# Optimization experiments

Measured on AMD Instinct MI355X. Metric: run time of the kernel, lower is better.

Reference implementation:

```python
import jax, jax.numpy as jnp
import numpy as np

B, H, S, F_RANK, D_HEAD = 1, 8, 4096, 64, 64
NEG = -1e9


def setup_inputs() -> dict:
    key = jax.random.key(0)
    k1, k2, k3, k4 = jax.random.split(key, 4)
    v = jax.random.normal(k1, (B, H, S, D_HEAD), dtype=jnp.float32)
    A1 = jax.random.normal(k2, (B, H, S, F_RANK), dtype=jnp.float32)
    A2 = jax.random.normal(k3, (B, H, F_RANK, S), dtype=jnp.float32)
    mask = jax.random.randint(k4, (B, 1, S, S), 0, 2, dtype=jnp.int32)
    return {"v": v, "A1": A1, "A2": A2, "mask": mask, "len_q": S}


def reference(v, A1, A2, mask, len_q):
    # Rank-f factorized scores: [B,H,len_q,len_q]
    scores = jnp.einsum('bhsf,bhft->bhst', A1[:, :, :len_q, :], A2[:, :, :, :len_q])
    scores = scores[:mask.shape[0]]
    # masked_fill(mask != 0, -1e9)
    scores = jnp.where(mask[:, :, :len_q, :len_q] != 0, jnp.float32(NEG), scores)
    attn = jax.nn.softmax(scores, axis=-1)  # dropout is identity in eval mode
    output = jnp.einsum('bhst,bhtd->bhsd', attn, v[:, :, :len_q, :])
    return (output, attn)
```

## Files before the change

### kernel.cpp

```cpp
#include <hip/hip_runtime.h>
#include <hip/hip_bf16.h>
#include <stdint.h>

#define S_LEN 4096
#define NHEAD 8
#define NEGV  (-1000000000.0f)
#define L2E   1.44269504088896340736f

typedef __attribute__((ext_vector_type(8))) short bf16x8;
typedef __attribute__((ext_vector_type(4))) float f32x4;
typedef unsigned short u16;
typedef unsigned int   u32;

#define MFMA16(a,b,c) __builtin_amdgcn_mfma_f32_16x16x32_bf16((a),(b),(c),0,0,0)
#define EXP2F(x) __builtin_amdgcn_exp2f((x))

__device__ __forceinline__ void gl_lds16(const void* g, void* l) {
  __builtin_amdgcn_global_load_lds((const __attribute__((address_space(1))) void*)g,
                                   (__attribute__((address_space(3))) void*)l, 16, 0, 0);
}

#define WS_A1HI 0u
#define WS_A1LO (4u<<20)
#define WS_A2HI (8u<<20)
#define WS_A2LO (12u<<20)
#define WS_VHI  (16u<<20)
#define WS_VLO  (20u<<20)
#define WS_BM   (24u<<20)

__global__ void pk_mask(const int* __restrict__ mask, u32* __restrict__ bmT) {
  const int sb = blockIdx.x >> 4;
  const int t  = (blockIdx.x & 15) * 256 + threadIdx.x;
  u32 w = 0;
  #pragma unroll
  for (int j = 0; j < 32; ++j)
    w |= (mask[(size_t)(sb * 32 + j) * S_LEN + t] != 0 ? 1u : 0u) << j;
  bmT[sb * S_LEN + t] = w;
}

__global__ void pk_split(const float* __restrict__ src, u16* __restrict__ hi, u16* __restrict__ lo) {
  const int i = blockIdx.x * 256 + threadIdx.x;
  float4 x = ((const float4*)src)[i];
  ushort4 hv, lv;
  #pragma unroll
  for (int j = 0; j < 4; ++j) {
    float xv = ((const float*)&x)[j];
    __hip_bfloat16 hb = __float2bfloat16(xv);
    float hf = __bfloat162float(hb);
    __hip_bfloat16 lb = __float2bfloat16(xv - hf);
    ((u16*)&hv)[j] = *(u16*)&hb;
    ((u16*)&lv)[j] = *(u16*)&lb;
  }
  ((ushort4*)hi)[i] = hv;
  ((ushort4*)lo)[i] = lv;
}

__global__ void pk_tsplit(const float* __restrict__ src, u16* __restrict__ hi, u16* __restrict__ lo,
                          int chunk_stride, int row_stride) {
  const int h = blockIdx.x >> 6, ci = blockIdx.x & 63;
  const float* base = src + (size_t)h * (S_LEN * 64) + (size_t)ci * chunk_stride;
  __shared__ float tile[64][65];
  const int jr = threadIdx.x & 63, ir = threadIdx.x >> 6;
  #pragma unroll
  for (int p = 0; p < 16; ++p) {
    int i = p * 4 + ir;
    tile[i][jr] = base[(size_t)i * row_stride + jr];
  }
  __syncthreads();
  const size_t ob = (size_t)(h * 64 + ci) * 4096;
  #pragma unroll
  for (int p = 0; p < 16; ++p) {
    int o = p * 256 + threadIdx.x;
    int r = o >> 6;
    int cc = (o & 63) ^ ((r & 7) << 3);
    float xv = tile[cc][r];
    __hip_bfloat16 hb = __float2bfloat16(xv);
    float hf = __bfloat162float(hb);
    __hip_bfloat16 lb = __float2bfloat16(xv - hf);
    hi[ob + o] = *(u16*)&hb;
    lo[ob + o] = *(u16*)&lb;
  }
}

__launch_bounds__(256, 2)
__global__ void fattn_main(const u16* __restrict__ a1hi, const u16* __restrict__ a1lo,
                           const u16* __restrict__ a2hi, const u16* __restrict__ a2lo,
                           const u16* __restrict__ vhi,  const u16* __restrict__ vlo,
                           const u32* __restrict__ bmT,  float* __restrict__ dout) {
  constexpr int TB = 128, NCH = S_LEN / TB;
  const int h   = blockIdx.x & 7;
  const int sb  = blockIdx.x >> 3;
  const int tid = threadIdx.x;
  const int w = tid >> 6, lane = tid & 63;
  const int g = lane >> 4, c = lane & 15;
  const int wsr = w >> 1;
  const int wth = w & 1;
  const int sbase = sb * 64 + wsr * 32;
  const int sb32  = sb * 2 + wsr;

  __shared__ __align__(16) char smem[76800];
  u16* st_a2h = (u16*)smem;
  u16* st_a2l = (u16*)(smem + 16384);
  u16* st_vh  = (u16*)(smem + 32768);
  u16* st_vl  = (u16*)(smem + 49152);
  u16* atb    = (u16*)(smem + 65536);
  float* mlm  = (float*)(smem + 75776);
  float* mll  = (float*)(smem + 75776 + 512);

  bf16x8 a1f[2][2][2];
  #pragma unroll
  for (int mt = 0; mt < 2; ++mt)
    #pragma unroll
    for (int kk = 0; kk < 2; ++kk) {
      size_t base = (size_t)(h * S_LEN + sbase + mt * 16 + c) * 64 + kk * 32 + g * 8;
      a1f[mt][kk][0] = *(const bf16x8*)(a1hi + base);
      a1f[mt][kk][1] = *(const bf16x8*)(a1lo + base);
    }

  float rm[2][4], rl[2][4];
  #pragma unroll
  for (int mt = 0; mt < 2; ++mt)
    #pragma unroll
    for (int r = 0; r < 4; ++r) { rm[mt][r] = -INFINITY; rl[mt][r] = 0.f; }

  const u32* bmrow = bmT + (size_t)sb32 * S_LEN;

  auto stage16 = [&](u16* dst, const u16* srcb) {
    const char* gsb = (const char*)srcb;
    #pragma unroll
    for (int i = 0; i < 4; ++i) {
      int blk = i * 4 + w;
      gl_lds16(gsb + blk * 1024 + lane * 16, (char*)dst + blk * 1024);
    }
  };

  auto compute_scores = [&](f32x4 (&acc)[2][4]) {
    #pragma unroll
    for (int kk = 0; kk < 2; ++kk)
      #pragma unroll
      for (int nt = 0; nt < 4; ++nt) {
        int eb = wth * 4096 + (nt * 16 + c) * 64 + ((kk * 32 + g * 8) ^ ((c & 7) << 3));
        bf16x8 bh = *(const bf16x8*)(st_a2h + eb);
        bf16x8 bl = *(const bf16x8*)(st_a2l + eb);
        #pragma unroll
        for (int mt = 0; mt < 2; ++mt) {
          acc[mt][nt] = MFMA16(a1f[mt][kk][0], bh, acc[mt][nt]);
          acc[mt][nt] = MFMA16(a1f[mt][kk][0], bl, acc[mt][nt]);
          acc[mt][nt] = MFMA16(a1f[mt][kk][1], bh, acc[mt][nt]);
        }
      }
  };

  #pragma unroll 1
  for (int ci = 0; ci < NCH; ++ci) {
    __syncthreads();
    stage16(st_a2h, a2hi + (size_t)(h * 64 + ci * 2) * 4096);
    stage16(st_a2l, a2lo + (size_t)(h * 64 + ci * 2) * 4096);
    __syncthreads();

    f32x4 acc[2][4];
    #pragma unroll
    for (int mt = 0; mt < 2; ++mt)
      #pragma unroll
      for (int nt = 0; nt < 4; ++nt) acc[mt][nt] = (f32x4){0.f, 0.f, 0.f, 0.f};
    compute_scores(acc);

    u32 mw[4];
    #pragma unroll
    for (int nt = 0; nt < 4; ++nt) mw[nt] = bmrow[ci * TB + wth * 64 + nt * 16 + c];

    float x[2][4][4];
    #pragma unroll
    for (int mt = 0; mt < 2; ++mt)
      #pragma unroll
      for (int nt = 0; nt < 4; ++nt)
        #pragma unroll
        for (int r = 0; r < 4; ++r) {
          float vs = acc[mt][nt][r] * L2E;
          x[mt][nt][r] = ((mw[nt] >> (mt * 16 + g * 4 + r)) & 1u) ? (NEGV * L2E) : vs;
        }

    #pragma unroll
    for (int mt = 0; mt < 2; ++mt)
      #pragma unroll
      for (int r = 0; r < 4; ++r) {
        float mx = fmaxf(fmaxf(x[mt][0][r], x[mt][1][r]), fmaxf(x[mt][2][r], x[mt][3][r]));
        #pragma unroll
        for (int off = 1; off < 16; off <<= 1) mx = fmaxf(mx, __shfl_xor(mx, off));
        float mo = rm[mt][r];
        float mn = fmaxf(mo, mx);
        float alpha = EXP2F(mo - mn);
        float sum = EXP2F(x[mt][0][r] - mn) + EXP2F(x[mt][1][r] - mn)
                  + EXP2F(x[mt][2][r] - mn) + EXP2F(x[mt][3][r] - mn);
        #pragma unroll
        for (int off = 1; off < 16; off <<= 1) sum += __shfl_xor(sum, off);
        rl[mt][r] = rl[mt][r] * alpha + sum;
        rm[mt][r] = mn;
      }
  }

  __syncthreads();
  if (c == 0) {
    #pragma unroll
    for (int mt = 0; mt < 2; ++mt)
      #pragma unroll
      for (int r = 0; r < 4; ++r) {
        mlm[w * 32 + mt * 16 + g * 4 + r] = rm[mt][r];
        mll[w * 32 + mt * 16 + g * 4 + r] = rl[mt][r];
      }
  }
  __syncthreads();
  #pragma unroll
  for (int mt = 0; mt < 2; ++mt)
    #pragma unroll
    for (int r = 0; r < 4; ++r) {
      int sl = mt * 16 + g * 4 + r;
      float m2 = mlm[(w ^ 1) * 32 + sl], l2 = mll[(w ^ 1) * 32 + sl];
      float mo = rm[mt][r];
      float M  = fmaxf(mo, m2);
      float L  = rl[mt][r] * EXP2F(mo - M) + l2 * EXP2F(m2 - M);
      rm[mt][r] = M;
      rl[mt][r] = 1.0f / L;
    }

  f32x4 oacc[2][4];
  #pragma unroll
  for (int mt = 0; mt < 2; ++mt)
    #pragma unroll
    for (int dt = 0; dt < 4; ++dt) oacc[mt][dt] = (f32x4){0.f, 0.f, 0.f, 0.f};

  float* aout = dout + (size_t)NHEAD * S_LEN * 64;

  #pragma unroll 1
  for (int ci = 0; ci < NCH; ++ci) {
    __syncthreads();
    stage16(st_a2h, a2hi + (size_t)(h * 64 + ci * 2) * 4096);
    stage16(st_a2l, a2lo + (size_t)(h * 64 + ci * 2) * 4096);
    stage16(st_vh,  vhi  + (size_t)(h * 64 + ci * 2) * 4096);
    stage16(st_vl,  vlo  + (size_t)(h * 64 + ci * 2) * 4096);
    __syncthreads();

    f32x4 acc[2][4];
    #pragma unroll
    for (int mt = 0; mt < 2; ++mt)
      #pragma unroll
      for (int nt = 0; nt < 4; ++nt) acc[mt][nt] = (f32x4){0.f, 0.f, 0.f, 0.f};
    compute_scores(acc);

    u32 mw[4];
    #pragma unroll
    for (int nt = 0; nt < 4; ++nt) mw[nt] = bmrow[ci * TB + wth * 64 + nt * 16 + c];

    f32x4 atn[2][4];
    #pragma unroll
    for (int mt = 0; mt < 2; ++mt)
      #pragma unroll
      for (int nt = 0; nt < 4; ++nt)
        #pragma unroll
        for (int r = 0; r < 4; ++r) {
          float vs = acc[mt][nt][r] * L2E;
          float xx = ((mw[nt] >> (mt * 16 + g * 4 + r)) & 1u) ? (NEGV * L2E) : vs;
          atn[mt][nt][r] = EXP2F(xx - rm[mt][r]) * rl[mt][r];
        }

    {
      size_t rowb = (size_t)(h * S_LEN + sbase) * S_LEN + ci * TB + wth * 64;
      #pragma unroll
      for (int mt = 0; mt < 2; ++mt)
        #pragma unroll
        for (int nt = 0; nt < 4; ++nt)
          #pragma unroll
          for (int r = 0; r < 4; ++r)
            aout[rowb + (size_t)(mt * 16 + g * 4 + r) * S_LEN + nt * 16 + c] = atn[mt][nt][r];
    }

    u16* myatb = atb + w * 1280;
    #pragma unroll
    for (int kk2 = 0; kk2 < 2; ++kk2) {
      #pragma unroll
      for (int mt = 0; mt < 2; ++mt)
        #pragma unroll
        for (int ntl = 0; ntl < 2; ++ntl)
          #pragma unroll
          for (int r = 0; r < 4; ++r) {
            __hip_bfloat16 hb = __float2bfloat16(atn[mt][kk2 * 2 + ntl][r]);
            myatb[(mt * 16 + g * 4 + r) * 40 + ntl * 16 + c] = *(u16*)&hb;
          }
      bf16x8 af[2];
      #pragma unroll
      for (int mt = 0; mt < 2; ++mt)
        af[mt] = *(const bf16x8*)(myatb + (mt * 16 + c) * 40 + g * 8);
      #pragma unroll
      for (int dt = 0; dt < 4; ++dt) {
        int ve = wth * 4096 + (dt * 16 + c) * 64 + ((kk2 * 32 + g * 8) ^ ((c & 7) << 3));
        bf16x8 bvh = *(const bf16x8*)(st_vh + ve);
        bf16x8 bvl = *(const bf16x8*)(st_vl + ve);
        #pragma unroll
        for (int mt = 0; mt < 2; ++mt) {
          oacc[mt][dt] = MFMA16(af[mt], bvh, oacc[mt][dt]);
          oacc[mt][dt] = MFMA16(af[mt], bvl, oacc[mt][dt]);
        }
      }
    }
  }

  __syncthreads();
  float* outx = (float*)smem;
  if (wth == 1) {
    #pragma unroll
    for (int mt = 0; mt < 2; ++mt)
      #pragma unroll
      for (int dt = 0; dt < 4; ++dt)
        #pragma unroll
        for (int r = 0; r < 4; ++r)
          outx[wsr * 2112 + (mt * 16 + g * 4 + r) * 66 + dt * 16 + c] = oacc[mt][dt][r];
  }
  __syncthreads();
  if (wth == 0) {
    #pragma unroll
    for (int mt = 0; mt < 2; ++mt)
      #pragma unroll
      for (int dt = 0; dt < 4; ++dt)
        #pragma unroll
        for (int r = 0; r < 4; ++r) {
          float vv = oacc[mt][dt][r] + outx[wsr * 2112 + (mt * 16 + g * 4 + r) * 66 + dt * 16 + c];
          int s = sbase + mt * 16 + g * 4 + r;
          dout[(size_t)(h * S_LEN + s) * 64 + dt * 16 + c] = vv;
        }
  }
}

extern "C" void kernel_launch(void* const* d_in, const int* in_sizes, int n_in,
                              void* d_out, int out_size, void* d_ws, size_t ws_size,
                              hipStream_t stream) {
  (void)in_sizes; (void)n_in; (void)out_size; (void)ws_size;
  const float* v    = (const float*)d_in[0];
  const float* A1   = (const float*)d_in[1];
  const float* A2   = (const float*)d_in[2];
  const int*   mask = (const int*)d_in[3];
  float* out = (float*)d_out;
  char* ws = (char*)d_ws;

  u16* a1hi = (u16*)(ws + WS_A1HI);
  u16* a1lo = (u16*)(ws + WS_A1LO);
  u16* a2hi = (u16*)(ws + WS_A2HI);
  u16* a2lo = (u16*)(ws + WS_A2LO);
  u16* vhi  = (u16*)(ws + WS_VHI);
  u16* vlo  = (u16*)(ws + WS_VLO);
  u32* bmT  = (u32*)(ws + WS_BM);

  pk_mask  <<<2048, 256, 0, stream>>>(mask, bmT);
  pk_split <<<2048, 256, 0, stream>>>(A1, a1hi, a1lo);
  pk_tsplit<<<512,  256, 0, stream>>>(A2, a2hi, a2lo, 64, 4096);
  pk_tsplit<<<512,  256, 0, stream>>>(v,  vhi,  vlo,  4096, 64);
  fattn_main<<<512, 256, 0, stream>>>(a1hi, a1lo, a2hi, a2lo, vhi, vlo, bmT, out);
}
```

Measured before the change: 801.7 us.

## Single-pass softmax without max, bf16 exp staging plus separate normalize kernel

Measured after the change: 807.8 us. No clear change (+0.8%).

```diff
diff --git a/kernel.cpp b/kernel.cpp
--- a/kernel.cpp
+++ b/kernel.cpp
@@ -4,7 +4,6 @@
 
 #define S_LEN 4096
 #define NHEAD 8
-#define NEGV  (-1000000000.0f)
 #define L2E   1.44269504088896340736f
 
 typedef __attribute__((ext_vector_type(8))) short bf16x8;
@@ -27,6 +26,8 @@
 #define WS_VHI  (16u<<20)
 #define WS_VLO  (20u<<20)
 #define WS_BM   (24u<<20)
+#define WS_INVL (26u<<20)
+#define WS_EXPB (28u<<20)
 
 __global__ void pk_mask(const int* __restrict__ mask, u32* __restrict__ bmT) {
   const int sb = blockIdx.x >> 4;
@@ -82,12 +83,12 @@
   }
 }
 
-__launch_bounds__(256, 2)
+__launch_bounds__(512, 2)
 __global__ void fattn_main(const u16* __restrict__ a1hi, const u16* __restrict__ a1lo,
                            const u16* __restrict__ a2hi, const u16* __restrict__ a2lo,
                            const u16* __restrict__ vhi,  const u16* __restrict__ vlo,
-                           const u32* __restrict__ bmT,  float* __restrict__ dout) {
-  constexpr int TB = 128, NCH = S_LEN / TB;
+                           const u32* __restrict__ bmT,  u16* __restrict__ expb,
+                           float* __restrict__ invl,     float* __restrict__ dout) {
   const int h   = blockIdx.x & 7;
   const int sb  = blockIdx.x >> 3;
   const int tid = threadIdx.x;
@@ -95,17 +96,12 @@
   const int g = lane >> 4, c = lane & 15;
   const int wsr = w >> 1;
   const int wth = w & 1;
-  const int sbase = sb * 64 + wsr * 32;
-  const int sb32  = sb * 2 + wsr;
-
-  __shared__ __align__(16) char smem[76800];
-  u16* st_a2h = (u16*)smem;
-  u16* st_a2l = (u16*)(smem + 16384);
-  u16* st_vh  = (u16*)(smem + 32768);
-  u16* st_vl  = (u16*)(smem + 49152);
-  u16* atb    = (u16*)(smem + 65536);
-  float* mlm  = (float*)(smem + 75776);
-  float* mll  = (float*)(smem + 75776 + 512);
+  const int sbase = sb * 128 + wsr * 32;
+  const int sb32  = sb * 4 + wsr;
+
+  __shared__ __align__(16) char smem[87040];
+  u16*   atb = (u16*)(smem + 65536);
+  float* mll = (float*)(smem + 86016);
 
   bf16x8 a1f[2][2][2];
   #pragma unroll
@@ -117,31 +113,49 @@
       a1f[mt][kk][1] = *(const bf16x8*)(a1lo + base);
     }
 
-  float rm[2][4], rl[2][4];
-  #pragma unroll
-  for (int mt = 0; mt < 2; ++mt)
-    #pragma unroll
-    for (int r = 0; r < 4; ++r) { rm[mt][r] = -INFINITY; rl[mt][r] = 0.f; }
+  float rl[2][4];
+  f32x4 oacc[2][4];
+  #pragma unroll
+  for (int mt = 0; mt < 2; ++mt) {
+    #pragma unroll
+    for (int r = 0; r < 4; ++r) rl[mt][r] = 0.f;
+    #pragma unroll
+    for (int dt = 0; dt < 4; ++dt) oacc[mt][dt] = (f32x4){0.f, 0.f, 0.f, 0.f};
+  }
 
   const u32* bmrow = bmT + (size_t)sb32 * S_LEN;
 
-  auto stage16 = [&](u16* dst, const u16* srcb) {
-    const char* gsb = (const char*)srcb;
-    #pragma unroll
-    for (int i = 0; i < 4; ++i) {
-      int blk = i * 4 + w;
-      gl_lds16(gsb + blk * 1024 + lane * 16, (char*)dst + blk * 1024);
-    }
+  auto stage_all = [&](int bufi, int ci) {
+    const size_t tb = (size_t)(h * 64 + ci) * 4096;
+    char* lb = smem + bufi * 32768;
+    const int off = w * 1024 + lane * 16;
+    gl_lds16((const char*)(a2hi + tb) + off, lb +         w * 1024);
+    gl_lds16((const char*)(a2lo + tb) + off, lb +  8192 + w * 1024);
+    gl_lds16((const char*)(vhi  + tb) + off, lb + 16384 + w * 1024);
+    gl_lds16((const char*)(vlo  + tb) + off, lb + 24576 + w * 1024);
   };
 
-  auto compute_scores = [&](f32x4 (&acc)[2][4]) {
+  stage_all(0, 0);
+  __syncthreads();
+
+  #pragma unroll 1
+  for (int ci = 0; ci < 64; ++ci) {
+    if (ci < 63) stage_all((ci + 1) & 1, ci + 1);
+
+    const u16* base = (const u16*)(smem + (ci & 1) * 32768);
+
+    f32x4 acc[2][2];
+    #pragma unroll
+    for (int mt = 0; mt < 2; ++mt)
+      #pragma unroll
+      for (int nt = 0; nt < 2; ++nt) acc[mt][nt] = (f32x4){0.f, 0.f, 0.f, 0.f};
     #pragma unroll
     for (int kk = 0; kk < 2; ++kk)
       #pragma unroll
-      for (int nt = 0; nt < 4; ++nt) {
-        int eb = wth * 4096 + (nt * 16 + c) * 64 + ((kk * 32 + g * 8) ^ ((c & 7) << 3));
-        bf16x8 bh = *(const bf16x8*)(st_a2h + eb);
-        bf16x8 bl = *(const bf16x8*)(st_a2l + eb);
+      for (int nt = 0; nt < 2; ++nt) {
+        int eb = (wth * 32 + nt * 16 + c) * 64 + ((kk * 32 + g * 8) ^ ((c & 7) << 3));
+        bf16x8 bh = *(const bf16x8*)(base + eb);
+        bf16x8 bl = *(const bf16x8*)(base + 4096 + eb);
         #pragma unroll
         for (int mt = 0; mt < 2; ++mt) {
           acc[mt][nt] = MFMA16(a1f[mt][kk][0], bh, acc[mt][nt]);
@@ -149,160 +163,99 @@
           acc[mt][nt] = MFMA16(a1f[mt][kk][1], bh, acc[mt][nt]);
         }
       }
-  };
-
-  #pragma unroll 1
-  for (int ci = 0; ci < NCH; ++ci) {
-    __syncthreads();
-    stage16(st_a2h, a2hi + (size_t)(h * 64 + ci * 2) * 4096);
-    stage16(st_a2l, a2lo + (size_t)(h * 64 + ci * 2) * 4096);
-    __syncthreads();
-
-    f32x4 acc[2][4];
-    #pragma unroll
-    for (int mt = 0; mt < 2; ++mt)
-      #pragma unroll
-      for (int nt = 0; nt < 4; ++nt) acc[mt][nt] = (f32x4){0.f, 0.f, 0.f, 0.f};
-    compute_scores(acc);
-
-    u32 mw[4];
-    #pragma unroll
-    for (int nt = 0; nt < 4; ++nt) mw[nt] = bmrow[ci * TB + wth * 64 + nt * 16 + c];
-
-    float x[2][4][4];
-    #pragma unroll
-    for (int mt = 0; mt < 2; ++mt)
-      #pragma unroll
-      for (int nt = 0; nt < 4; ++nt)
+
+    const u32 mw0 = bmrow[ci * 64 + wth * 32 + c];
+    const u32 mw1 = bmrow[ci * 64 + wth * 32 + 16 + c];
+    float e[2][2][4];
+    #pragma unroll
+    for (int mt = 0; mt < 2; ++mt)
+      #pragma unroll
+      for (int nt = 0; nt < 2; ++nt) {
+        const u32 mwv = nt ? mw1 : mw0;
         #pragma unroll
         for (int r = 0; r < 4; ++r) {
-          float vs = acc[mt][nt][r] * L2E;
-          x[mt][nt][r] = ((mw[nt] >> (mt * 16 + g * 4 + r)) & 1u) ? (NEGV * L2E) : vs;
-        }
-
-    #pragma unroll
-    for (int mt = 0; mt < 2; ++mt)
-      #pragma unroll
-      for (int r = 0; r < 4; ++r) {
-        float mx = fmaxf(fmaxf(x[mt][0][r], x[mt][1][r]), fmaxf(x[mt][2][r], x[mt][3][r]));
-        #pragma unroll
-        for (int off = 1; off < 16; off <<= 1) mx = fmaxf(mx, __shfl_xor(mx, off));
-        float mo = rm[mt][r];
-        float mn = fmaxf(mo, mx);
-        float alpha = EXP2F(mo - mn);
-        float sum = EXP2F(x[mt][0][r] - mn) + EXP2F(x[mt][1][r] - mn)
-                  + EXP2F(x[mt][2][r] - mn) + EXP2F(x[mt][3][r] - mn);
-        #pragma unroll
-        for (int off = 1; off < 16; off <<= 1) sum += __shfl_xor(sum, off);
-        rl[mt][r] = rl[mt][r] * alpha + sum;
-        rm[mt][r] = mn;
-      }
-  }
-
-  __syncthreads();
-  if (c == 0) {
-    #pragma unroll
-    for (int mt = 0; mt < 2; ++mt)
-      #pragma unroll
-      for (int r = 0; r < 4; ++r) {
-        mlm[w * 32 + mt * 16 + g * 4 + r] = rm[mt][r];
-        mll[w * 32 + mt * 16 + g * 4 + r] = rl[mt][r];
-      }
-  }
-  __syncthreads();
-  #pragma unroll
-  for (int mt = 0; mt < 2; ++mt)
-    #pragma unroll
-    for (int r = 0; r < 4; ++r) {
-      int sl = mt * 16 + g * 4 + r;
-      float m2 = mlm[(w ^ 1) * 32 + sl], l2 = mll[(w ^ 1) * 32 + sl];
-      float mo = rm[mt][r];
-      float M  = fmaxf(mo, m2);
-      float L  = rl[mt][r] * EXP2F(mo - M) + l2 * EXP2F(m2 - M);
-      rm[mt][r] = M;
-      rl[mt][r] = 1.0f / L;
-    }
-
-  f32x4 oacc[2][4];
-  #pragma unroll
-  for (int mt = 0; mt < 2; ++mt)
-    #pragma unroll
-    for (int dt = 0; dt < 4; ++dt) oacc[mt][dt] = (f32x4){0.f, 0.f, 0.f, 0.f};
-
-  float* aout = dout + (size_t)NHEAD * S_LEN * 64;
-
-  #pragma unroll 1
-  for (int ci = 0; ci < NCH; ++ci) {
-    __syncthreads();
-    stage16(st_a2h, a2hi + (size_t)(h * 64 + ci * 2) * 4096);
-    stage16(st_a2l, a2lo + (size_t)(h * 64 + ci * 2) * 4096);
-    stage16(st_vh,  vhi  + (size_t)(h * 64 + ci * 2) * 4096);
-    stage16(st_vl,  vlo  + (size_t)(h * 64 + ci * 2) * 4096);
-    __syncthreads();
-
-    f32x4 acc[2][4];
-    #pragma unroll
-    for (int mt = 0; mt < 2; ++mt)
-      #pragma unroll
-      for (int nt = 0; nt < 4; ++nt) acc[mt][nt] = (f32x4){0.f, 0.f, 0.f, 0.f};
-    compute_scores(acc);
-
-    u32 mw[4];
-    #pragma unroll
-    for (int nt = 0; nt < 4; ++nt) mw[nt] = bmrow[ci * TB + wth * 64 + nt * 16 + c];
-
-    f32x4 atn[2][4];
-    #pragma unroll
-    for (int mt = 0; mt < 2; ++mt)
-      #pragma unroll
-      for (int nt = 0; nt < 4; ++nt)
-        #pragma unroll
-        for (int r = 0; r < 4; ++r) {
-          float vs = acc[mt][nt][r] * L2E;
-          float xx = ((mw[nt] >> (mt * 16 + g * 4 + r)) & 1u) ? (NEGV * L2E) : vs;
-          atn[mt][nt][r] = EXP2F(xx - rm[mt][r]) * rl[mt][r];
-        }
-
-    {
-      size_t rowb = (size_t)(h * S_LEN + sbase) * S_LEN + ci * TB + wth * 64;
-      #pragma unroll
-      for (int mt = 0; mt < 2; ++mt)
-        #pragma unroll
-        for (int nt = 0; nt < 4; ++nt)
-          #pragma unroll
-          for (int r = 0; r < 4; ++r)
-            aout[rowb + (size_t)(mt * 16 + g * 4 + r) * S_LEN + nt * 16 + c] = atn[mt][nt][r];
-    }
-
-    u16* myatb = atb + w * 1280;
-    #pragma unroll
-    for (int kk2 = 0; kk2 < 2; ++kk2) {
-      #pragma unroll
-      for (int mt = 0; mt < 2; ++mt)
-        #pragma unroll
-        for (int ntl = 0; ntl < 2; ++ntl)
-          #pragma unroll
-          for (int r = 0; r < 4; ++r) {
-            __hip_bfloat16 hb = __float2bfloat16(atn[mt][kk2 * 2 + ntl][r]);
-            myatb[(mt * 16 + g * 4 + r) * 40 + ntl * 16 + c] = *(u16*)&hb;
-          }
-      bf16x8 af[2];
-      #pragma unroll
-      for (int mt = 0; mt < 2; ++mt)
-        af[mt] = *(const bf16x8*)(myatb + (mt * 16 + c) * 40 + g * 8);
-      #pragma unroll
-      for (int dt = 0; dt < 4; ++dt) {
-        int ve = wth * 4096 + (dt * 16 + c) * 64 + ((kk2 * 32 + g * 8) ^ ((c & 7) << 3));
-        bf16x8 bvh = *(const bf16x8*)(st_vh + ve);
-        bf16x8 bvl = *(const bf16x8*)(st_vl + ve);
-        #pragma unroll
-        for (int mt = 0; mt < 2; ++mt) {
-          oacc[mt][dt] = MFMA16(af[mt], bvh, oacc[mt][dt]);
-          oacc[mt][dt] = MFMA16(af[mt], bvl, oacc[mt][dt]);
+          float ex = EXP2F(acc[mt][nt][r] * L2E);
+          float ev = ((mwv >> (mt * 16 + g * 4 + r)) & 1u) ? 0.f : ex;
+          e[mt][nt][r] = ev;
+          rl[mt][r] += ev;
         }
       }
+
+    u16* my = atb + w * 1280;
+    #pragma unroll
+    for (int mt = 0; mt < 2; ++mt)
+      #pragma unroll
+      for (int nt = 0; nt < 2; ++nt)
+        #pragma unroll
+        for (int r = 0; r < 4; ++r) {
+          __hip_bfloat16 hb = __float2bfloat16(e[mt][nt][r]);
+          my[(mt * 16 + g * 4 + r) * 40 + nt * 16 + c] = *(u16*)&hb;
+        }
+    bf16x8 af[2];
+    #pragma unroll
+    for (int mt = 0; mt < 2; ++mt)
+      af[mt] = *(const bf16x8*)(my + (mt * 16 + c) * 40 + g * 8);
+
+    #pragma unroll
+    for (int mt = 0; mt < 2; ++mt)
+      *(bf16x8*)(expb + (size_t)(h * S_LEN + sbase + mt * 16 + c) * S_LEN
+                       + ci * 64 + wth * 32 + g * 8) = af[mt];
+
+    #pragma unroll
+    for (int dt = 0; dt < 4; ++dt) {
+      int ve = (dt * 16 + c) * 64 + ((wth * 32 + g * 8) ^ ((c & 7) << 3));
+      bf16x8 bvh = *(const bf16x8*)(base + 8192 + ve);
+      bf16x8 bvl = *(const bf16x8*)(base + 12288 + ve);
+      #pragma unroll
+      for (int mt = 0; mt < 2; ++mt) {
+        oacc[mt][dt] = MFMA16(af[mt], bvh, oacc[mt][dt]);
+        oacc[mt][dt] = MFMA16(af[mt], bvl, oacc[mt][dt]);
+      }
     }
-  }
+
+    __syncthreads();
+  }
+
+  #pragma unroll
+  for (int mt = 0; mt < 2; ++mt)
+    #pragma unroll
+    for (int r = 0; r < 4; ++r) {
+      float s = rl[mt][r];
+      #pragma unroll
+      for (int off = 1; off < 16; off <<= 1) s += __shfl_xor(s, off);
+      rl[mt][r] = s;
+    }
+  __syncthreads();
+  if (c == 0) {
+    #pragma unroll
+    for (int mt = 0; mt < 2; ++mt)
+      #pragma unroll
+      for (int r = 0; r < 4; ++r)
+        mll[w * 32 + mt * 16 + g * 4 + r] = rl[mt][r];
+  }
+  __syncthreads();
+  float inv[2][4];
+  #pragma unroll
+  for (int mt = 0; mt < 2; ++mt)
+    #pragma unroll
+    for (int r = 0; r < 4; ++r) {
+      float tot = rl[mt][r] + mll[(w ^ 1) * 32 + mt * 16 + g * 4 + r];
+      inv[mt][r] = 1.0f / tot;
+    }
+  if (wth == 0 && c == 0) {
+    #pragma unroll
+    for (int mt = 0; mt < 2; ++mt)
+      #pragma unroll
+      for (int r = 0; r < 4; ++r)
+        invl[h * S_LEN + sbase + mt * 16 + g * 4 + r] = inv[mt][r];
+  }
+  #pragma unroll
+  for (int mt = 0; mt < 2; ++mt)
+    #pragma unroll
+    for (int dt = 0; dt < 4; ++dt)
+      #pragma unroll
+      for (int r = 0; r < 4; ++r)
+        oacc[mt][dt][r] *= inv[mt][r];
 
   __syncthreads();
   float* outx = (float*)smem;
@@ -328,6 +281,26 @@
           dout[(size_t)(h * S_LEN + s) * 64 + dt * 16 + c] = vv;
         }
   }
+}
+
+__global__ void attn_norm(const u16* __restrict__ expb, const float* __restrict__ invl,
+                          float* __restrict__ aout) {
+  const int row = blockIdx.x;
+  const float iv = invl[row];
+  const u16* src = expb + (size_t)row * S_LEN;
+  float* dst = aout + (size_t)row * S_LEN;
+  const int t0 = threadIdx.x * 16;
+  bf16x8 v0 = *(const bf16x8*)(src + t0);
+  bf16x8 v1 = *(const bf16x8*)(src + t0 + 8);
+  float4 o[4];
+  #pragma unroll
+  for (int j = 0; j < 8; ++j) {
+    ((float*)o)[j]     = __uint_as_float(((u32)(u16)v0[j]) << 16) * iv;
+    ((float*)o)[j + 8] = __uint_as_float(((u32)(u16)v1[j]) << 16) * iv;
+  }
+  #pragma unroll
+  for (int k = 0; k < 4; ++k)
+    ((float4*)(dst + t0))[k] = o[k];
 }
 
 extern "C" void kernel_launch(void* const* d_in, const int* in_sizes, int n_in,
@@ -348,10 +321,15 @@
   u16* vhi  = (u16*)(ws + WS_VHI);
   u16* vlo  = (u16*)(ws + WS_VLO);
   u32* bmT  = (u32*)(ws + WS_BM);
+  float* invl = (float*)(ws + WS_INVL);
+  u16* expb = (u16*)(ws + WS_EXPB);
+
+  float* aout = out + (size_t)NHEAD * S_LEN * 64;
 
   pk_mask  <<<2048, 256, 0, stream>>>(mask, bmT);
   pk_split <<<2048, 256, 0, stream>>>(A1, a1hi, a1lo);
   pk_tsplit<<<512,  256, 0, stream>>>(A2, a2hi, a2lo, 64, 4096);
   pk_tsplit<<<512,  256, 0, stream>>>(v,  vhi,  vlo,  4096, 64);
-  fattn_main<<<512, 256, 0, stream>>>(a1hi, a1lo, a2hi, a2lo, vhi, vlo, bmT, out);
-}
+  fattn_main<<<256, 512, 0, stream>>>(a1hi, a1lo, a2hi, a2lo, vhi, vlo, bmT, expb, invl, out);
+  attn_norm<<<NHEAD * S_LEN, 256, 0, stream>>>(expb, invl, aout);
+}
```
